# Performance work log

Measured on AMD Instinct MI355X. Metric: run time of the kernel, lower is better.

The kernel has to match this reference:

```python
import jax, jax.numpy as jnp
import numpy as np

WS = 9
PAD = WS // 2  # 4


def _unfold(x, H, W):
    # x: [N,C,H,W] -> [N,C,81,H,W], reflect-padded 9x9 windows,
    # tap order (row-major over kernel) matching torch F.unfold.
    xp = jnp.pad(x, ((0, 0), (0, 0), (PAD, PAD), (PAD, PAD)), mode='reflect')
    return jnp.stack(
        [xp[:, :, i:i + H, j:j + W] for i in range(WS) for j in range(WS)],
        axis=2,
    )


def _bilinear_align_corners(x, H, W):
    # torch F.interpolate(mode='bilinear', align_corners=True)
    N, C, h, w = x.shape
    ys = jnp.linspace(0.0, h - 1.0, H)
    xs = jnp.linspace(0.0, w - 1.0, W)
    y0 = jnp.floor(ys).astype(jnp.int32)
    x0 = jnp.floor(xs).astype(jnp.int32)
    y1 = jnp.minimum(y0 + 1, h - 1)
    x1 = jnp.minimum(x0 + 1, w - 1)
    wy = (ys - y0)[:, None]   # [H,1]
    wx = (xs - x0)[None, :]   # [1,W]
    g = lambda yi, xi: x[:, :, yi, :][:, :, :, xi]
    top = g(y0, x0) * (1.0 - wx) + g(y0, x1) * wx
    bot = g(y1, x0) * (1.0 - wx) + g(y1, x1) * wx
    return top * (1.0 - wy) + bot * wy


def setup_inputs() -> dict:
    key = jax.random.key(0)
    ks = jax.random.split(key, 6)
    N, H, W = 4, 128, 128
    return {
        'delta': jax.random.normal(ks[0], (N, 64, H, W), jnp.float32),
        'out': jax.random.normal(ks[1], (N, 2, H // 2, W // 2), jnp.float32),
        'ab_logits': jax.random.normal(ks[2], (N, 81, H * W), jnp.float32),
        'w1': jax.random.normal(ks[3], (16, 64), jnp.float32) * 0.125,
        'b1': jnp.zeros((16,), jnp.float32),
        'w2': jax.random.normal(ks[4], (16, 64), jnp.float32) * 0.125,
        'b2': jnp.zeros((16,), jnp.float32),
        'gamma_d': jnp.ones((), jnp.float32),
        'gamma_s': jnp.ones((), jnp.float32),
    }


def reference(delta, out, ab_logits, w1, b1, w2, b2, gamma_d, gamma_s):
    N, C, H, W = delta.shape
    # 1x1 convs
    f1 = jnp.einsum('nchw,oc->nohw', delta, w1) + b1[None, :, None, None]
    f2 = jnp.einsum('nchw,oc->nohw', delta, w2) + b2[None, :, None, None]
    # windowed squared-distance correlation
    f2_unf = _unfold(f2, H, W).reshape(N, 16, WS * WS, H * W)
    d_center = f1.reshape(N, 16, 1, H * W)
    delta_logits = -jnp.sum((d_center - f2_unf) ** 2, axis=1)  # [N,81,HW]
    attn = jax.nn.softmax(gamma_d * delta_logits + gamma_s * ab_logits, axis=1)
    # weighted local aggregation of (detached, upsampled) out
    out_up = _bilinear_align_corners(jax.lax.stop_gradient(out), H, W)
    out_unf = _unfold(out_up, H, W).reshape(N, 2, WS * WS, H * W)
    out_refine = jnp.sum(out_unf * attn[:, None], axis=2)  # [N,2,HW]
    return out_refine.reshape(N, 2, H, W)
```

## Files before the change

### kernel.cpp

```cpp
#include <hip/hip_runtime.h>

#define HW   16384
#define NPIX 65536

typedef _Float16 f16x2 __attribute__((ext_vector_type(2)));

#if __has_builtin(__builtin_amdgcn_fdot2)
#define DOT2(a, b, c) __builtin_amdgcn_fdot2((a), (b), (c), false)
#else
__device__ __forceinline__ float dot2_fb(f16x2 a, f16x2 b, float c) {
    return fmaf((float)a.x, (float)b.x, fmaf((float)a.y, (float)b.y, c));
}
#define DOT2(a, b, c) dot2_fb((a), (b), (c))
#endif

#if __has_builtin(__builtin_amdgcn_exp2f)
#define EXP2F(x) __builtin_amdgcn_exp2f(x)
#else
#define EXP2F(x) exp2f(x)
#endif

__device__ __forceinline__ unsigned packh2(float a, float b) {
    f16x2 h; h.x = (_Float16)a; h.y = (_Float16)b;
    return __builtin_bit_cast(unsigned, h);
}
__device__ __forceinline__ f16x2 bch(unsigned u) {
    return __builtin_bit_cast(f16x2, u);
}

__global__ __launch_bounds__(256) void pass1_kernel(
    const float* __restrict__ delta, const float* __restrict__ outlo,
    const float* __restrict__ w1, const float* __restrict__ b1,
    const float* __restrict__ w2, const float* __restrict__ b2,
    uint4* __restrict__ f1p4, uint4* __restrict__ f2p4, float2* __restrict__ recp)
{
    const int m = blockIdx.y;
    const int g = blockIdx.x * 256 + threadIdx.x;
    const int n = g >> 14;
    const int p = g & (HW - 1);

    const float* __restrict__ wm = m ? w2 : w1;
    const float* __restrict__ bm = m ? b2 : b1;

    float d[64];
    const float* db = delta + (size_t)n * 64 * HW + p;
#pragma unroll
    for (int c = 0; c < 64; ++c) d[c] = db[(size_t)c * HW];

    float acc[16];
#pragma unroll
    for (int o = 0; o < 16; ++o) {
        float a = bm[o];
        const float* wr = wm + o * 64;
#pragma unroll
        for (int c = 0; c < 64; ++c) a = fmaf(wr[c], d[c], a);
        acc[o] = a;
    }

    uint4* dst = m ? f2p4 : f1p4;
    uint4 q;
    q.x = packh2(acc[0], acc[1]);   q.y = packh2(acc[2], acc[3]);
    q.z = packh2(acc[4], acc[5]);   q.w = packh2(acc[6], acc[7]);
    dst[g] = q;
    q.x = packh2(acc[8], acc[9]);   q.y = packh2(acc[10], acc[11]);
    q.z = packh2(acc[12], acc[13]); q.w = packh2(acc[14], acc[15]);
    dst[NPIX + g] = q;

    if (m) {
        float f2sq = 0.f;
#pragma unroll
        for (int o = 0; o < 16; ++o) f2sq = fmaf(acc[o], acc[o], f2sq);

        const int y = p >> 7, x = p & 127;
        const float ys = (float)(y * 63) / 127.0f;
        const float xs = (float)(x * 63) / 127.0f;
        const int iy0 = (int)ys, ix0 = (int)xs;
        const float fy = ys - (float)iy0, fx = xs - (float)ix0;
        const int iy1 = min(iy0 + 1, 63), ix1 = min(ix0 + 1, 63);
        const float* ob = outlo + n * 2 * 4096;
        float o01[2];
#pragma unroll
        for (int cc = 0; cc < 2; ++cc) {
            const float* oc = ob + cc * 4096;
            const float v00 = oc[iy0*64+ix0], v01 = oc[iy0*64+ix1];
            const float v10 = oc[iy1*64+ix0], v11 = oc[iy1*64+ix1];
            const float top = v00 + fx * (v01 - v00);
            const float bot = v10 + fx * (v11 - v10);
            o01[cc] = top + fy * (bot - top);
        }
        float2 rc;
        rc.x = __builtin_bit_cast(float, packh2(o01[0], o01[1]));
        rc.y = f2sq;
        recp[g] = rc;
    }
}

__global__ __launch_bounds__(256) void pass2_kernel(
    const uint4* __restrict__ f1p4, const uint4* __restrict__ f2p4,
    const float2* __restrict__ recp, const float* __restrict__ ab,
    const float* __restrict__ gdp, const float* __restrict__ gsp,
    float* __restrict__ outp)
{
    __shared__ uint4  shA[384];
    __shared__ uint4  shB[384];
    __shared__ float2 shC[384];
    __shared__ float  shP[6 * 4 * 64];

    const int t = threadIdx.x;
    const int n = blockIdx.z;
    const int bx = blockIdx.x * 16, by = blockIdx.y * 8;

#pragma unroll
    for (int s = 0; s < 2; ++s) {
        const int idx = t + s * 256;
        if (idx < 384) {
            const int hy = idx / 24, hx = idx - hy * 24;
            int gy = by - 4 + hy; gy = gy < 0 ? -gy : (gy > 127 ? 254 - gy : gy);
            int gx = bx - 4 + hx; gx = gx < 0 ? -gx : (gx > 127 ? 254 - gx : gx);
            const int gg = n * HW + gy * 128 + gx;
            shA[idx] = f2p4[gg];
            shB[idx] = f2p4[NPIX + gg];
            shC[idx] = recp[gg];
        }
    }
    __syncthreads();

    const float gd = gdp[0], gs = gsp[0];
    const float L2E = 1.44269504088896f;
    const float g2 = 2.0f * gd * L2E, mg = -gd * L2E, gsl = gs * L2E;

    const int wh = t >> 6;
    const int l  = t & 63;
    const int px = l & 15, pyr = l >> 4;
    const int p0 = (by + pyr * 2) * 128 + bx + px;
    const int g0 = n * HW + p0;

    f16x2 f1a[8], f1b[8];
    {
        const uint4 A0 = f1p4[g0],       A1 = f1p4[NPIX + g0];
        const uint4 B0 = f1p4[g0 + 128], B1 = f1p4[NPIX + g0 + 128];
        f1a[0]=bch(A0.x); f1a[1]=bch(A0.y); f1a[2]=bch(A0.z); f1a[3]=bch(A0.w);
        f1a[4]=bch(A1.x); f1a[5]=bch(A1.y); f1a[6]=bch(A1.z); f1a[7]=bch(A1.w);
        f1b[0]=bch(B0.x); f1b[1]=bch(B0.y); f1b[2]=bch(B0.z); f1b[3]=bch(B0.w);
        f1b[4]=bch(B1.x); f1b[5]=bch(B1.y); f1b[6]=bch(B1.z); f1b[7]=bch(B1.w);
    }
    float f1sqa = 0.f, f1sqb = 0.f;
#pragma unroll
    for (int k = 0; k < 8; ++k) {
        f1sqa = DOT2(f1a[k], f1a[k], f1sqa);
        f1sqb = DOT2(f1b[k], f1b[k], f1sqb);
    }
    const float c0a = mg * f1sqa;
    const float c0b = mg * f1sqb;

    float s0 = 0.f, x00 = 0.f, x01 = 0.f;
    float s1 = 0.f, x10 = 0.f, x11 = 0.f;

    const float* abn = ab + (size_t)n * 81 * HW;
    const int nrows = (wh < 2) ? 3 : 2;

    for (int r = 0; r < nrows; ++r) {
        const int dyc = wh + r * 4;
        const bool has0 = (dyc <= 8);
        const bool has1 = (dyc >= 1);
        float a0v[9], a1v[9];
        if (has0) {
            const float* a0p = abn + (size_t)(dyc * 9) * HW + p0;
#pragma unroll
            for (int j = 0; j < 9; ++j) a0v[j] = a0p[(size_t)j * HW];
        }
        if (has1) {
            const float* a1p = abn + (size_t)((dyc - 1) * 9) * HW + p0 + 128;
#pragma unroll
            for (int j = 0; j < 9; ++j) a1v[j] = a1p[(size_t)j * HW];
        }
        const int rib = (pyr * 2 + dyc) * 24 + px;
#pragma unroll
        for (int j = 0; j < 9; ++j) {
            const uint4  q0 = shA[rib + j];
            const uint4  q1 = shB[rib + j];
            const float2 rc = shC[rib + j];
            f16x2 v0 = bch(q0.x), v1 = bch(q0.y), v2 = bch(q0.z), v3 = bch(q0.w);
            f16x2 v4 = bch(q1.x), v5 = bch(q1.y), v6 = bch(q1.z), v7 = bch(q1.w);
            const f16x2 oh = bch(__builtin_bit_cast(unsigned, rc.x));
            const float o0f = (float)oh.x, o1f = (float)oh.y;
            const float f2s = rc.y;
            if (has0) {
                float dt = DOT2(f1a[0], v0, 0.f);
                dt = DOT2(f1a[1], v1, dt); dt = DOT2(f1a[2], v2, dt);
                dt = DOT2(f1a[3], v3, dt); dt = DOT2(f1a[4], v4, dt);
                dt = DOT2(f1a[5], v5, dt); dt = DOT2(f1a[6], v6, dt);
                dt = DOT2(f1a[7], v7, dt);
                float e = fmaf(g2, dt, c0a);
                e = fmaf(mg, f2s, e);
                e = fmaf(gsl, a0v[j], e);
                const float w = EXP2F(e);
                s0 += w; x00 = fmaf(w, o0f, x00); x01 = fmaf(w, o1f, x01);
            }
            if (has1) {
                float dt = DOT2(f1b[0], v0, 0.f);
                dt = DOT2(f1b[1], v1, dt); dt = DOT2(f1b[2], v2, dt);
                dt = DOT2(f1b[3], v3, dt); dt = DOT2(f1b[4], v4, dt);
                dt = DOT2(f1b[5], v5, dt); dt = DOT2(f1b[6], v6, dt);
                dt = DOT2(f1b[7], v7, dt);
                float e = fmaf(g2, dt, c0b);
                e = fmaf(mg, f2s, e);
                e = fmaf(gsl, a1v[j], e);
                const float w = EXP2F(e);
                s1 += w; x10 = fmaf(w, o0f, x10); x11 = fmaf(w, o1f, x11);
            }
        }
    }

    shP[(0 * 4 + wh) * 64 + l] = s0;
    shP[(1 * 4 + wh) * 64 + l] = x00;
    shP[(2 * 4 + wh) * 64 + l] = x01;
    shP[(3 * 4 + wh) * 64 + l] = s1;
    shP[(4 * 4 + wh) * 64 + l] = x10;
    shP[(5 * 4 + wh) * 64 + l] = x11;
    __syncthreads();

    if (t < 64) {
        float v[6];
#pragma unroll
        for (int k = 0; k < 6; ++k) {
            const float* pp = &shP[k * 256 + t];
            v[k] = (pp[0] + pp[64]) + (pp[128] + pp[192]);
        }
        const int qx = t & 15, qyr = t >> 4;
        const int pp0 = (by + qyr * 2) * 128 + bx + qx;
        const float i0 = 1.0f / v[0], i1 = 1.0f / v[3];
        float* o0 = outp + (size_t)(n * 2 + 0) * HW;
        float* o1 = outp + (size_t)(n * 2 + 1) * HW;
        o0[pp0]       = v[1] * i0;
        o1[pp0]       = v[2] * i0;
        o0[pp0 + 128] = v[4] * i1;
        o1[pp0 + 128] = v[5] * i1;
    }
}

extern "C" void kernel_launch(void* const* d_in, const int* in_sizes, int n_in,
                              void* d_out, int out_size, void* d_ws, size_t ws_size,
                              hipStream_t stream) {
    const float* delta = (const float*)d_in[0];
    const float* outlo = (const float*)d_in[1];
    const float* ab    = (const float*)d_in[2];
    const float* w1    = (const float*)d_in[3];
    const float* b1    = (const float*)d_in[4];
    const float* w2    = (const float*)d_in[5];
    const float* b2    = (const float*)d_in[6];
    const float* gd    = (const float*)d_in[7];
    const float* gs    = (const float*)d_in[8];
    float* outp = (float*)d_out;

    uint4*  f1p4 = (uint4*)d_ws;
    uint4*  f2p4 = f1p4 + (size_t)2 * NPIX;
    float2* recp = (float2*)(f2p4 + (size_t)2 * NPIX);

    pass1_kernel<<<dim3(256, 2), dim3(256), 0, stream>>>(delta, outlo, w1, b1, w2, b2,
                                                         f1p4, f2p4, recp);
    pass2_kernel<<<dim3(8, 16, 4), dim3(256), 0, stream>>>(f1p4, f2p4, recp, ab,
                                                           gd, gs, outp);
}
```

Baseline: 112.0 us.

## Widen pass2 tiles to 64x4 with 512 threads and prefetch ab logits early

Pass2 now uses 512-thread blocks covering 64x4 output pixels, so each wavefront handles a full 64-pixel row pair. The halo overhead per tile drops from 24x12 for 16x8 outputs to 72x12 for 64x4 outputs. All ab_logits values for every row, plus the f1 features, are loaded into registers before the shared-memory fill and the barrier, so their global latency overlaps the halo staging. The cost is much higher register pressure from holding 54 prefetched floats per thread, which together with the 512-thread launch bound may cut occupancy or cause spills. The grid also shrinks to 256 blocks.

```diff
diff --git a/kernel.cpp b/kernel.cpp
--- a/kernel.cpp
+++ b/kernel.cpp
@@ -95,26 +95,57 @@
     }
 }
 
-__global__ __launch_bounds__(256) void pass2_kernel(
+__global__ __launch_bounds__(512) void pass2_kernel(
     const uint4* __restrict__ f1p4, const uint4* __restrict__ f2p4,
     const float2* __restrict__ recp, const float* __restrict__ ab,
     const float* __restrict__ gdp, const float* __restrict__ gsp,
     float* __restrict__ outp)
 {
-    __shared__ uint4  shA[384];
-    __shared__ uint4  shB[384];
-    __shared__ float2 shC[384];
-    __shared__ float  shP[6 * 4 * 64];
+    __shared__ uint4  shA[12 * 72];
+    __shared__ uint4  shB[12 * 72];
+    __shared__ float2 shC[12 * 72];
+    __shared__ float  shP[6 * 4 * 128];
 
     const int t = threadIdx.x;
     const int n = blockIdx.z;
-    const int bx = blockIdx.x * 16, by = blockIdx.y * 8;
+    const int bx = blockIdx.x * 64, by = blockIdx.y * 4;
+
+    const int w   = t >> 6;
+    const int wh  = w & 3;
+    const int pyr = w >> 2;
+    const int px  = t & 63;
+    const int pairid = pyr * 64 + px;
+    const int p0 = (by + pyr * 2) * 128 + bx + px;
+    const int g0 = n * HW + p0;
+
+    const float* abn = ab + (size_t)n * 81 * HW;
+    const int nrows = (wh < 2) ? 3 : 2;
+    float a0v[3][9], a1v[3][9];
+#pragma unroll
+    for (int r = 0; r < 3; ++r) {
+        if (r < nrows) {
+            const int dyc = wh + r * 4;
+            if (dyc <= 8) {
+                const float* pp = abn + (size_t)(dyc * 9) * HW + p0;
+#pragma unroll
+                for (int j = 0; j < 9; ++j) a0v[r][j] = pp[(size_t)j * HW];
+            }
+            if (dyc >= 1) {
+                const float* pp = abn + (size_t)((dyc - 1) * 9) * HW + p0 + 128;
+#pragma unroll
+                for (int j = 0; j < 9; ++j) a1v[r][j] = pp[(size_t)j * HW];
+            }
+        }
+    }
+
+    const uint4 A0 = f1p4[g0],       A1 = f1p4[NPIX + g0];
+    const uint4 B0 = f1p4[g0 + 128], B1 = f1p4[NPIX + g0 + 128];
 
 #pragma unroll
     for (int s = 0; s < 2; ++s) {
-        const int idx = t + s * 256;
-        if (idx < 384) {
-            const int hy = idx / 24, hx = idx - hy * 24;
+        const int idx = t + s * 512;
+        if (idx < 864) {
+            const int hy = idx / 72, hx = idx - hy * 72;
             int gy = by - 4 + hy; gy = gy < 0 ? -gy : (gy > 127 ? 254 - gy : gy);
             int gx = bx - 4 + hx; gx = gx < 0 ? -gx : (gx > 127 ? 254 - gx : gx);
             const int gg = n * HW + gy * 128 + gx;
@@ -129,21 +160,11 @@
     const float L2E = 1.44269504088896f;
     const float g2 = 2.0f * gd * L2E, mg = -gd * L2E, gsl = gs * L2E;
 
-    const int wh = t >> 6;
-    const int l  = t & 63;
-    const int px = l & 15, pyr = l >> 4;
-    const int p0 = (by + pyr * 2) * 128 + bx + px;
-    const int g0 = n * HW + p0;
-
     f16x2 f1a[8], f1b[8];
-    {
-        const uint4 A0 = f1p4[g0],       A1 = f1p4[NPIX + g0];
-        const uint4 B0 = f1p4[g0 + 128], B1 = f1p4[NPIX + g0 + 128];
-        f1a[0]=bch(A0.x); f1a[1]=bch(A0.y); f1a[2]=bch(A0.z); f1a[3]=bch(A0.w);
-        f1a[4]=bch(A1.x); f1a[5]=bch(A1.y); f1a[6]=bch(A1.z); f1a[7]=bch(A1.w);
-        f1b[0]=bch(B0.x); f1b[1]=bch(B0.y); f1b[2]=bch(B0.z); f1b[3]=bch(B0.w);
-        f1b[4]=bch(B1.x); f1b[5]=bch(B1.y); f1b[6]=bch(B1.z); f1b[7]=bch(B1.w);
-    }
+    f1a[0]=bch(A0.x); f1a[1]=bch(A0.y); f1a[2]=bch(A0.z); f1a[3]=bch(A0.w);
+    f1a[4]=bch(A1.x); f1a[5]=bch(A1.y); f1a[6]=bch(A1.z); f1a[7]=bch(A1.w);
+    f1b[0]=bch(B0.x); f1b[1]=bch(B0.y); f1b[2]=bch(B0.z); f1b[3]=bch(B0.w);
+    f1b[4]=bch(B1.x); f1b[5]=bch(B1.y); f1b[6]=bch(B1.z); f1b[7]=bch(B1.w);
     float f1sqa = 0.f, f1sqb = 0.f;
 #pragma unroll
     for (int k = 0; k < 8; ++k) {
@@ -156,78 +177,67 @@
     float s0 = 0.f, x00 = 0.f, x01 = 0.f;
     float s1 = 0.f, x10 = 0.f, x11 = 0.f;
 
-    const float* abn = ab + (size_t)n * 81 * HW;
-    const int nrows = (wh < 2) ? 3 : 2;
-
-    for (int r = 0; r < nrows; ++r) {
-        const int dyc = wh + r * 4;
-        const bool has0 = (dyc <= 8);
-        const bool has1 = (dyc >= 1);
-        float a0v[9], a1v[9];
-        if (has0) {
-            const float* a0p = abn + (size_t)(dyc * 9) * HW + p0;
-#pragma unroll
-            for (int j = 0; j < 9; ++j) a0v[j] = a0p[(size_t)j * HW];
-        }
-        if (has1) {
-            const float* a1p = abn + (size_t)((dyc - 1) * 9) * HW + p0 + 128;
-#pragma unroll
-            for (int j = 0; j < 9; ++j) a1v[j] = a1p[(size_t)j * HW];
-        }
-        const int rib = (pyr * 2 + dyc) * 24 + px;
-#pragma unroll
-        for (int j = 0; j < 9; ++j) {
-            const uint4  q0 = shA[rib + j];
-            const uint4  q1 = shB[rib + j];
-            const float2 rc = shC[rib + j];
-            f16x2 v0 = bch(q0.x), v1 = bch(q0.y), v2 = bch(q0.z), v3 = bch(q0.w);
-            f16x2 v4 = bch(q1.x), v5 = bch(q1.y), v6 = bch(q1.z), v7 = bch(q1.w);
-            const f16x2 oh = bch(__builtin_bit_cast(unsigned, rc.x));
-            const float o0f = (float)oh.x, o1f = (float)oh.y;
-            const float f2s = rc.y;
-            if (has0) {
-                float dt = DOT2(f1a[0], v0, 0.f);
-                dt = DOT2(f1a[1], v1, dt); dt = DOT2(f1a[2], v2, dt);
-                dt = DOT2(f1a[3], v3, dt); dt = DOT2(f1a[4], v4, dt);
-                dt = DOT2(f1a[5], v5, dt); dt = DOT2(f1a[6], v6, dt);
-                dt = DOT2(f1a[7], v7, dt);
-                float e = fmaf(g2, dt, c0a);
-                e = fmaf(mg, f2s, e);
-                e = fmaf(gsl, a0v[j], e);
-                const float w = EXP2F(e);
-                s0 += w; x00 = fmaf(w, o0f, x00); x01 = fmaf(w, o1f, x01);
+#pragma unroll
+    for (int r = 0; r < 3; ++r) {
+        if (r < nrows) {
+            const int dyc = wh + r * 4;
+            const bool has0 = (dyc <= 8);
+            const bool has1 = (dyc >= 1);
+            const int rib = (pyr * 2 + dyc) * 72 + px;
+#pragma unroll
+            for (int j = 0; j < 9; ++j) {
+                const uint4  q0 = shA[rib + j];
+                const uint4  q1 = shB[rib + j];
+                const float2 rc = shC[rib + j];
+                const f16x2 v0 = bch(q0.x), v1 = bch(q0.y), v2 = bch(q0.z), v3 = bch(q0.w);
+                const f16x2 v4 = bch(q1.x), v5 = bch(q1.y), v6 = bch(q1.z), v7 = bch(q1.w);
+                const f16x2 oh = bch(__builtin_bit_cast(unsigned, rc.x));
+                const float o0f = (float)oh.x, o1f = (float)oh.y;
+                const float f2s = rc.y;
+                if (has0) {
+                    float dt = DOT2(f1a[0], v0, 0.f);
+                    dt = DOT2(f1a[1], v1, dt); dt = DOT2(f1a[2], v2, dt);
+                    dt = DOT2(f1a[3], v3, dt); dt = DOT2(f1a[4], v4, dt);
+                    dt = DOT2(f1a[5], v5, dt); dt = DOT2(f1a[6], v6, dt);
+                    dt = DOT2(f1a[7], v7, dt);
+                    float e = fmaf(g2, dt, c0a);
+                    e = fmaf(mg, f2s, e);
+                    e = fmaf(gsl, a0v[r][j], e);
+                    const float wgt = EXP2F(e);
+                    s0 += wgt; x00 = fmaf(wgt, o0f, x00); x01 = fmaf(wgt, o1f, x01);
+                }
+                if (has1) {
+                    float dt = DOT2(f1b[0], v0, 0.f);
+                    dt = DOT2(f1b[1], v1, dt); dt = DOT2(f1b[2], v2, dt);
+                    dt = DOT2(f1b[3], v3, dt); dt = DOT2(f1b[4], v4, dt);
+                    dt = DOT2(f1b[5], v5, dt); dt = DOT2(f1b[6], v6, dt);
+                    dt = DOT2(f1b[7], v7, dt);
+                    float e = fmaf(g2, dt, c0b);
+                    e = fmaf(mg, f2s, e);
+                    e = fmaf(gsl, a1v[r][j], e);
+                    const float wgt = EXP2F(e);
+                    s1 += wgt; x10 = fmaf(wgt, o0f, x10); x11 = fmaf(wgt, o1f, x11);
+                }
             }
-            if (has1) {
-                float dt = DOT2(f1b[0], v0, 0.f);
-                dt = DOT2(f1b[1], v1, dt); dt = DOT2(f1b[2], v2, dt);
-                dt = DOT2(f1b[3], v3, dt); dt = DOT2(f1b[4], v4, dt);
-                dt = DOT2(f1b[5], v5, dt); dt = DOT2(f1b[6], v6, dt);
-                dt = DOT2(f1b[7], v7, dt);
-                float e = fmaf(g2, dt, c0b);
-                e = fmaf(mg, f2s, e);
-                e = fmaf(gsl, a1v[j], e);
-                const float w = EXP2F(e);
-                s1 += w; x10 = fmaf(w, o0f, x10); x11 = fmaf(w, o1f, x11);
-            }
-        }
-    }
-
-    shP[(0 * 4 + wh) * 64 + l] = s0;
-    shP[(1 * 4 + wh) * 64 + l] = x00;
-    shP[(2 * 4 + wh) * 64 + l] = x01;
-    shP[(3 * 4 + wh) * 64 + l] = s1;
-    shP[(4 * 4 + wh) * 64 + l] = x10;
-    shP[(5 * 4 + wh) * 64 + l] = x11;
+        }
+    }
+
+    shP[(0 * 4 + wh) * 128 + pairid] = s0;
+    shP[(1 * 4 + wh) * 128 + pairid] = x00;
+    shP[(2 * 4 + wh) * 128 + pairid] = x01;
+    shP[(3 * 4 + wh) * 128 + pairid] = s1;
+    shP[(4 * 4 + wh) * 128 + pairid] = x10;
+    shP[(5 * 4 + wh) * 128 + pairid] = x11;
     __syncthreads();
 
-    if (t < 64) {
+    if (t < 128) {
         float v[6];
 #pragma unroll
         for (int k = 0; k < 6; ++k) {
-            const float* pp = &shP[k * 256 + t];
-            v[k] = (pp[0] + pp[64]) + (pp[128] + pp[192]);
-        }
-        const int qx = t & 15, qyr = t >> 4;
+            const float* pp = &shP[k * 512 + t];
+            v[k] = (pp[0] + pp[128]) + (pp[256] + pp[384]);
+        }
+        const int qx = t & 63, qyr = t >> 6;
         const int pp0 = (by + qyr * 2) * 128 + bx + qx;
         const float i0 = 1.0f / v[0], i1 = 1.0f / v[3];
         float* o0 = outp + (size_t)(n * 2 + 0) * HW;
@@ -259,6 +269,6 @@
 
     pass1_kernel<<<dim3(256, 2), dim3(256), 0, stream>>>(delta, outlo, w1, b1, w2, b2,
                                                          f1p4, f2p4, recp);
-    pass2_kernel<<<dim3(8, 16, 4), dim3(256), 0, stream>>>(f1p4, f2p4, recp, ab,
+    pass2_kernel<<<dim3(2, 32, 4), dim3(512), 0, stream>>>(f1p4, f2p4, recp, ab,
                                                            gd, gs, outp);
 }
```

Result: no change. 114.0 us (+1.9%).
